# Kernel tuning notes

Measured on AMD Instinct MI355X. Metric: run time of the kernel, lower is better.

Reference implementation:

```python
import jax, jax.numpy as jnp
import numpy as np

N, T, P = 4096, 4096, 12  # series, timesteps, seasonality period


def setup_inputs() -> dict:
    key = jax.random.key(0)
    ks = jax.random.split(key, 8)
    return {
        "alpha": jax.random.uniform(ks[0], (N,), dtype=jnp.float32),
        "beta": jax.random.uniform(ks[1], (N,), dtype=jnp.float32),
        "gamma": jax.random.uniform(ks[2], (N,), dtype=jnp.float32),
        "init_level": jax.random.normal(ks[3], (N,), dtype=jnp.float32),
        "init_trend": jax.random.normal(ks[4], (N,), dtype=jnp.float32) * 0.01,
        "init_seasonal": jax.random.normal(ks[5], (N, P), dtype=jnp.float32),
        "obs_noise": jax.random.normal(ks[6], (N, T), dtype=jnp.float32),
        "err": jax.random.normal(ks[7], (N, T), dtype=jnp.float32),
    }


def reference(alpha, beta, gamma, init_level, init_trend, init_seasonal, obs_noise, err):
    """ETS 'AAA' (additive error/trend/seasonal) recurrence, vectorized over N series.

    Per timestep t (matching the torch loop with model_type='AAA'):
      current = level + trend + seasonal[t % P]
      y[t]    = current + obs_noise[t] * 0.1
      level'  = alpha*(current + err[t]) + (1-alpha)*(level + trend)
      trend'  = beta*(level' - level) + (1-beta)*trend
      seasonal[t % P] = gamma*err[t] + (1-gamma)*seasonal[t % P]
    """
    Tlen = obs_noise.shape[1]
    Pn = init_seasonal.shape[1]

    def step(carry, xs):
        level, trend, seasonal = carry  # (N,), (N,), (N, P)
        t, on, e = xs                   # scalar, (N,), (N,)
        idx = t % Pn
        s_t = seasonal[:, idx]
        current = level + trend + s_t
        y = current + on * 0.1
        new_level = alpha * (current + e) + (1.0 - alpha) * (level + trend)
        new_trend = beta * (new_level - level) + (1.0 - beta) * trend
        new_seasonal = seasonal.at[:, idx].set(gamma * e + (1.0 - gamma) * s_t)
        return (new_level, new_trend, new_seasonal), y

    xs = (jnp.arange(Tlen), obs_noise.T, err.T)  # scan over time
    _, ys = jax.lax.scan(step, (init_level, init_trend, init_seasonal), xs)
    return ys.T  # (N, T)
```

## Files before the change

### kernel.cpp

```cpp
#include <hip/hip_runtime.h>

#define DEV static __device__ __forceinline__

#define SKEW(j) ((j) + ((j) >> 5))

__global__ __launch_bounds__(128) void ets_w2(
    const float* __restrict__ alpha_, const float* __restrict__ beta_,
    const float* __restrict__ gamma_, const float* __restrict__ lvl0,
    const float* __restrict__ tr0, const float* __restrict__ seas0,
    const float* __restrict__ obs, const float* __restrict__ err,
    float* __restrict__ out, int T)
{
  __shared__ float er_s[4224];
  __shared__ float tot[20];

  const int n = blockIdx.x;
  const int tid = threadIdx.x;
  const int lane = tid & 63;
  const int wv = tid >> 6;

  const float4* ER4 = reinterpret_cast<const float4*>(err + (size_t)n * T);
  const float4* OB4 = reinterpret_cast<const float4*>(obs + (size_t)n * T);
  const int nf4 = T >> 2;

  for (int i = tid; i < nf4; i += 128) {
    float4 e = ER4[i];
    int j = i << 2;
    er_s[SKEW(j + 0)] = e.x; er_s[SKEW(j + 1)] = e.y;
    er_s[SKEW(j + 2)] = e.z; er_s[SKEW(j + 3)] = e.w;
  }

  const float a = alpha_[n], b = beta_[n], g = gamma_[n];
  const float ab = a * b, ig = 1.0f - g;

  const int nper = T / 12;
  const int base = nper >> 7, rem = nper & 127;
  const int m  = base + (tid < rem ? 1 : 0);
  const int p0 = tid * base + min(tid, rem);
  const int t0 = p0 * 12;

  __syncthreads();

  float l = 0.f, tr = 0.f, s[12];
#pragma unroll
  for (int j = 0; j < 12; ++j) s[j] = 0.f;
  {
    int t = t0;
    for (int u = 0; u < m; ++u, t += 12) {
#pragma unroll
      for (int j = 0; j < 12; ++j) {
        float e = er_s[SKEW(t + j)];
        float se = s[j] + e;
        float lt = l + tr;
        l  = fmaf(a, se, lt);
        tr = fmaf(ab, se, tr);
        s[j] = fmaf(g, e, ig * s[j]);
      }
    }
  }

  float S0 = 0.f, S1 = 0.f, dk = 1.f;
  for (int k = 0; k < m; ++k) { S0 += dk; S1 += (float)k * dk; dk *= ig; }
  float GL = 12.0f * (float)m;
  float Gd = dk;
  float Gf = ab * S0;
  float GA = fmaf(a, S0, ab * ((GL - 1.0f) * S0 - 12.0f * S1));
  float Pl = l, Pt = tr, Ps[12];
#pragma unroll
  for (int j = 0; j < 12; ++j) Ps[j] = s[j];

#pragma unroll
  for (int dlt = 1; dlt < 64; dlt <<= 1) {
    float oL  = __shfl_up(GL, dlt, 64);
    float od  = __shfl_up(Gd, dlt, 64);
    float of  = __shfl_up(Gf, dlt, 64);
    float oA  = __shfl_up(GA, dlt, 64);
    float oPl = __shfl_up(Pl, dlt, 64);
    float oPt = __shfl_up(Pt, dlt, 64);
    float oPs[12];
#pragma unroll
    for (int j = 0; j < 12; ++j) oPs[j] = __shfl_up(Ps[j], dlt, 64);
    if (lane >= dlt) {
      float S = 0.f, W = 0.f;
#pragma unroll
      for (int j = 0; j < 12; ++j) {
        S += oPs[j];
        W = fmaf((float)j, oPs[j], W);
      }
      float dot = GA * S - Gf * W;
      float nPl = oPl + GL * oPt + dot + Pl;
      float nPt = fmaf(Gf, S, oPt) + Pt;
#pragma unroll
      for (int j = 0; j < 12; ++j) Ps[j] = fmaf(Gd, oPs[j], Ps[j]);
      GA = oA + GL * of + GA * od;
      Pl = nPl; Pt = nPt;
      Gf = of + Gf * od;
      Gd = od * Gd;
      GL = oL + GL;
    }
  }

  if (wv == 0 && lane == 63) {
    tot[0] = GL; tot[1] = Gd; tot[2] = Gf; tot[3] = GA; tot[4] = Pl; tot[5] = Pt;
#pragma unroll
    for (int j = 0; j < 12; ++j) tot[6 + j] = Ps[j];
  }
  __syncthreads();

  float xl = lvl0[n], xt = tr0[n], xs[12];
#pragma unroll
  for (int j = 0; j < 12; ++j) xs[j] = seas0[(size_t)n * 12 + j];
  if (wv == 1) {
    float ss = 0.f, sw = 0.f;
#pragma unroll
    for (int j = 0; j < 12; ++j) {
      ss += xs[j];
      sw = fmaf((float)j, xs[j], sw);
    }
    float cdot = tot[3] * ss - tot[2] * sw;
    float nxl = xl + tot[0] * xt + cdot + tot[4];
    float nxt = fmaf(tot[2], ss, xt) + tot[5];
#pragma unroll
    for (int j = 0; j < 12; ++j) xs[j] = fmaf(tot[1], xs[j], tot[6 + j]);
    xl = nxl; xt = nxt;
  }

  float ss = 0.f, sw = 0.f;
#pragma unroll
  for (int j = 0; j < 12; ++j) {
    ss += xs[j];
    sw = fmaf((float)j, xs[j], sw);
  }
  float cdot = GA * ss - Gf * sw;
  float yl = xl + GL * xt + cdot + Pl;
  float yt = fmaf(Gf, ss, xt) + Pt;
  float ys[12];
#pragma unroll
  for (int j = 0; j < 12; ++j) ys[j] = fmaf(Gd, xs[j], Ps[j]);

  l  = __shfl_up(yl, 1, 64);
  tr = __shfl_up(yt, 1, 64);
#pragma unroll
  for (int j = 0; j < 12; ++j) s[j] = __shfl_up(ys[j], 1, 64);
  if (lane == 0) {
    l = xl; tr = xt;
#pragma unroll
    for (int j = 0; j < 12; ++j) s[j] = xs[j];
  }

  {
    int t = t0;
    for (int u = 0; u < m; ++u, t += 12) {
#pragma unroll
      for (int j = 0; j < 12; ++j) {
        int ad = SKEW(t + j);
        float e = er_s[ad];
        float lt = l + tr;
        float cur = lt + s[j];
        er_s[ad] = cur;
        float se = s[j] + e;
        l  = fmaf(a, se, lt);
        tr = fmaf(ab, se, tr);
        s[j] = fmaf(g, e, ig * s[j]);
      }
    }
  }
  if (tid == 127) {
    int tt = nper * 12;
    int tail = T - tt;
#pragma unroll
    for (int j = 0; j < 11; ++j) {
      if (j < tail) {
        int ad = SKEW(tt + j);
        float e = er_s[ad];
        float lt = l + tr;
        float cur = lt + s[j];
        er_s[ad] = cur;
        float se = s[j] + e;
        l  = fmaf(a, se, lt);
        tr = fmaf(ab, se, tr);
        s[j] = fmaf(g, e, ig * s[j]);
      }
    }
  }

  __syncthreads();

  float4* Y4 = reinterpret_cast<float4*>(out + (size_t)n * T);
  for (int i = tid; i < nf4; i += 128) {
    float4 o = OB4[i];
    int j = i << 2;
    float4 v = make_float4(fmaf(o.x, 0.1f, er_s[SKEW(j + 0)]),
                           fmaf(o.y, 0.1f, er_s[SKEW(j + 1)]),
                           fmaf(o.z, 0.1f, er_s[SKEW(j + 2)]),
                           fmaf(o.w, 0.1f, er_s[SKEW(j + 3)]));
    Y4[i] = v;
  }
}

__global__ void ets_gen(
    const float* __restrict__ alpha_, const float* __restrict__ beta_,
    const float* __restrict__ gamma_, const float* __restrict__ lvl0,
    const float* __restrict__ tr0, const float* __restrict__ seas0,
    const float* __restrict__ obs, const float* __restrict__ err,
    float* __restrict__ out, int N, int T, int P)
{
  extern __shared__ float smem[];
  int n = blockIdx.x * blockDim.x + threadIdx.x;
  if (n >= N) return;
  float* s = smem + (size_t)threadIdx.x * P;
  for (int j = 0; j < P; ++j) s[j] = seas0[(size_t)n * P + j];

  float a = alpha_[n], b = beta_[n], g = gamma_[n];
  float ia = 1.0f - a, ib = 1.0f - b, ig = 1.0f - g;
  float level = lvl0[n], trend = tr0[n];

  const float* on = obs + (size_t)n * T;
  const float* er = err + (size_t)n * T;
  float*       yo = out + (size_t)n * T;

  int idx = 0;
  for (int t = 0; t < T; ++t) {
    float onj = on[t], ej = er[t];
    float sj  = s[idx];
    float cur = level + trend + sj;
    yo[t] = fmaf(onj, 0.1f, cur);
    float lt  = level + trend;
    float nl  = fmaf(a, cur + ej, ia * lt);
    float nt  = fmaf(b, nl - level, ib * trend);
    s[idx]    = fmaf(g, ej, ig * sj);
    level = nl; trend = nt;
    if (++idx == P) idx = 0;
  }
}

extern "C" void kernel_launch(void* const* d_in, const int* in_sizes, int n_in,
                              void* d_out, int out_size, void* d_ws, size_t ws_size,
                              hipStream_t stream) {
  (void)n_in; (void)out_size; (void)d_ws; (void)ws_size;
  const float* alpha = (const float*)d_in[0];
  const float* beta  = (const float*)d_in[1];
  const float* gamma = (const float*)d_in[2];
  const float* lvl0  = (const float*)d_in[3];
  const float* tr0   = (const float*)d_in[4];
  const float* seas0 = (const float*)d_in[5];
  const float* obs   = (const float*)d_in[6];
  const float* err   = (const float*)d_in[7];
  float* y = (float*)d_out;

  int N = in_sizes[0];
  int P = in_sizes[5] / N;
  int T = in_sizes[6] / N;

  if (P == 12 && (T % 4) == 0 && T >= 12 && T <= 4096) {
    ets_w2<<<dim3(N), dim3(128), 0, stream>>>(
        alpha, beta, gamma, lvl0, tr0, seas0, obs, err, y, T);
  } else {
    int bs = 64;
    size_t sh = (size_t)bs * (size_t)P * sizeof(float);
    ets_gen<<<dim3((N + bs - 1) / bs), dim3(bs), sh, stream>>>(
        alpha, beta, gamma, lvl0, tr0, seas0, obs, err, y, N, T, P);
  }
}
```

Baseline: 44.32 us.

## Vectorize shared-memory accesses and prefetch observation noise into registers early

The per-element skewed shared-memory layout becomes a float4-aligned layout with padding every 128 floats, so staging, both scan passes and the output pass use 128-bit LDS loads and stores instead of scalar ones. The obs_noise row is also loaded into registers at kernel start (8 float4 per thread), so the global read overlaps the scan instead of sitting on the critical path at the end. The costs are higher register pressure from the 8 float4 buffers and possible bank conflicts from the new padding pattern when threads access strided 12-element chunks.

```diff
diff --git a/kernel.cpp b/kernel.cpp
--- a/kernel.cpp
+++ b/kernel.cpp
@@ -2,7 +2,24 @@
 
 #define DEV static __device__ __forceinline__
 
-#define SKEW(j) ((j) + ((j) >> 5))
+#define SKEW4(j) ((j) + (((j) >> 7) << 2))
+
+DEV float elem(const float4& v, int j) {
+  switch (j & 3) {
+    case 0: return v.x;
+    case 1: return v.y;
+    case 2: return v.z;
+    default: return v.w;
+  }
+}
+DEV void setelem(float4& v, int j, float x) {
+  switch (j & 3) {
+    case 0: v.x = x; break;
+    case 1: v.y = x; break;
+    case 2: v.z = x; break;
+    default: v.w = x; break;
+  }
+}
 
 __global__ __launch_bounds__(128) void ets_w2(
     const float* __restrict__ alpha_, const float* __restrict__ beta_,
@@ -11,7 +28,7 @@
     const float* __restrict__ obs, const float* __restrict__ err,
     float* __restrict__ out, int T)
 {
-  __shared__ float er_s[4224];
+  __shared__ __align__(16) float er_s[4224];
   __shared__ float tot[20];
 
   const int n = blockIdx.x;
@@ -25,9 +42,14 @@
 
   for (int i = tid; i < nf4; i += 128) {
     float4 e = ER4[i];
-    int j = i << 2;
-    er_s[SKEW(j + 0)] = e.x; er_s[SKEW(j + 1)] = e.y;
-    er_s[SKEW(j + 2)] = e.z; er_s[SKEW(j + 3)] = e.w;
+    *reinterpret_cast<float4*>(&er_s[SKEW4(i << 2)]) = e;
+  }
+
+  float4 O[8];
+#pragma unroll
+  for (int k = 0; k < 8; ++k) {
+    int i = tid + (k << 7);
+    if (i < nf4) O[k] = OB4[i];
   }
 
   const float a = alpha_[n], b = beta_[n], g = gamma_[n];
@@ -47,9 +69,12 @@
   {
     int t = t0;
     for (int u = 0; u < m; ++u, t += 12) {
+      float4 e0 = *reinterpret_cast<const float4*>(&er_s[SKEW4(t)]);
+      float4 e1 = *reinterpret_cast<const float4*>(&er_s[SKEW4(t + 4)]);
+      float4 e2 = *reinterpret_cast<const float4*>(&er_s[SKEW4(t + 8)]);
 #pragma unroll
       for (int j = 0; j < 12; ++j) {
-        float e = er_s[SKEW(t + j)];
+        float e = elem(j < 4 ? e0 : (j < 8 ? e1 : e2), j);
         float se = s[j] + e;
         float lt = l + tr;
         l  = fmaf(a, se, lt);
@@ -151,9 +176,33 @@
   {
     int t = t0;
     for (int u = 0; u < m; ++u, t += 12) {
+      float4* a0 = reinterpret_cast<float4*>(&er_s[SKEW4(t)]);
+      float4* a1 = reinterpret_cast<float4*>(&er_s[SKEW4(t + 4)]);
+      float4* a2 = reinterpret_cast<float4*>(&er_s[SKEW4(t + 8)]);
+      float4 e0 = *a0, e1 = *a1, e2 = *a2;
+      float4 y0, y1, y2;
 #pragma unroll
       for (int j = 0; j < 12; ++j) {
-        int ad = SKEW(t + j);
+        float e = elem(j < 4 ? e0 : (j < 8 ? e1 : e2), j);
+        float lt = l + tr;
+        float cur = lt + s[j];
+        float4& yd = (j < 4 ? y0 : (j < 8 ? y1 : y2));
+        setelem(yd, j, cur);
+        float se = s[j] + e;
+        l  = fmaf(a, se, lt);
+        tr = fmaf(ab, se, tr);
+        s[j] = fmaf(g, e, ig * s[j]);
+      }
+      *a0 = y0; *a1 = y1; *a2 = y2;
+    }
+  }
+  if (tid == 127) {
+    int tt = nper * 12;
+    int tail = T - tt;
+#pragma unroll
+    for (int j = 0; j < 11; ++j) {
+      if (j < tail) {
+        int ad = SKEW4(tt + j);
         float e = er_s[ad];
         float lt = l + tr;
         float cur = lt + s[j];
@@ -165,36 +214,18 @@
       }
     }
   }
-  if (tid == 127) {
-    int tt = nper * 12;
-    int tail = T - tt;
-#pragma unroll
-    for (int j = 0; j < 11; ++j) {
-      if (j < tail) {
-        int ad = SKEW(tt + j);
-        float e = er_s[ad];
-        float lt = l + tr;
-        float cur = lt + s[j];
-        er_s[ad] = cur;
-        float se = s[j] + e;
-        l  = fmaf(a, se, lt);
-        tr = fmaf(ab, se, tr);
-        s[j] = fmaf(g, e, ig * s[j]);
-      }
-    }
-  }
 
   __syncthreads();
 
   float4* Y4 = reinterpret_cast<float4*>(out + (size_t)n * T);
-  for (int i = tid; i < nf4; i += 128) {
-    float4 o = OB4[i];
-    int j = i << 2;
-    float4 v = make_float4(fmaf(o.x, 0.1f, er_s[SKEW(j + 0)]),
-                           fmaf(o.y, 0.1f, er_s[SKEW(j + 1)]),
-                           fmaf(o.z, 0.1f, er_s[SKEW(j + 2)]),
-                           fmaf(o.w, 0.1f, er_s[SKEW(j + 3)]));
-    Y4[i] = v;
+#pragma unroll
+  for (int k = 0; k < 8; ++k) {
+    int i = tid + (k << 7);
+    if (i < nf4) {
+      float4 c = *reinterpret_cast<const float4*>(&er_s[SKEW4(i << 2)]);
+      Y4[i] = make_float4(fmaf(O[k].x, 0.1f, c.x), fmaf(O[k].y, 0.1f, c.y),
+                          fmaf(O[k].z, 0.1f, c.z), fmaf(O[k].w, 0.1f, c.w));
+    }
   }
 }
 
```

Result: no change. 44.86 us (+1.2%).
